# Kernel optimization log

Hardware: AMD Instinct MI355X
Metric: run time of the kernel (lower is better)

The kernel has to match this reference:

```python
import jax, jax.numpy as jnp
import numpy as np

BN_EPS = 1e-5
KNN_K = 9
HEAD = 4


def _bn(x, gamma, beta, axis=1):
    # eval-mode BatchNorm with running_mean=0, running_var=1
    shape = [1] * x.ndim
    shape[axis] = -1
    scale = (gamma / jnp.sqrt(1.0 + BN_EPS)).reshape(shape)
    return x * scale + beta.reshape(shape)


def _conv1d(x, W, b):
    # 1x1 Conv1d == channel matmul; x: [B,C,N], W: [O,C], b: [O]
    return jnp.einsum('oc,bcn->bon', W, x) + b[None, :, None]


def _knn_idx(x, k):
    # x: [B,C,N] -> idx [B,N,k] of k nearest (incl. self)
    xx = jnp.sum(x * x, axis=1)                      # [B,N]
    inner = jnp.einsum('bcn,bcm->bnm', x, x)         # [B,N,N]
    neg_d = 2.0 * inner - xx[:, :, None] - xx[:, None, :]
    return jax.lax.top_k(neg_d, k)[1]


def _graph_feature(x, k):
    # x: [B,C,N] -> [B,2C,N,k]  (cat of center feature and center - neighbor)
    B, C, N = x.shape
    idx = _knn_idx(x, k)                             # [B,N,k]
    xt = jnp.transpose(x, (0, 2, 1))                 # [B,N,C]
    nbr = jax.vmap(lambda xb, ib: xb[ib])(xt, idx)   # [B,N,k,C]
    ctr = jnp.broadcast_to(xt[:, :, None, :], (B, N, k, C))
    feat = jnp.concatenate([ctr, ctr - nbr], axis=3)  # [B,N,k,2C]
    return jnp.transpose(feat, (0, 3, 1, 2))


def _dgcnn_max(x, w1, b1, g1, be1, w2, b2, g2, be2, k):
    # x: [B,C,N] -> [B,C,N]; two 1x1 convs + BN + ReLU then max over k
    ef = _graph_feature(x, k)                        # [B,2C,N,k]
    h = jnp.einsum('oc,bcnk->bonk', w1, ef) + b1[None, :, None, None]
    h = jax.nn.relu(_bn(h, g1, be1, axis=1))
    h = jnp.einsum('oc,bcnk->bonk', w2, h) + b2[None, :, None, None]
    h = jax.nn.relu(_bn(h, g2, be2, axis=1))
    return jnp.max(h, axis=-1)                       # [B,C,N]


def _attention(m1, m2, wq, bq, wk, bk, wv, bv, wmh, bmh, wc1, bc1, cg, cbe, wc2, bc2):
    B, C, N = m1.shape
    hd = C // HEAD
    q = _conv1d(m1, wq, bq).reshape(B, HEAD, hd, N)
    kk = _conv1d(m2, wk, bk).reshape(B, HEAD, hd, -1)
    v = _conv1d(m2, wv, bv).reshape(B, HEAD, hd, -1)
    score = jax.nn.softmax(jnp.einsum('bhdn,bhdm->bhnm', q, kk) / (float(hd) ** 0.5), axis=-1)
    add = jnp.einsum('bhnm,bhdm->bhdn', score, v).reshape(B, C, N)
    add = _conv1d(add, wmh, bmh)
    cat = jnp.concatenate([m1, add], axis=1)         # [B,2C,N]
    h = jax.nn.relu(_bn(_conv1d(cat, wc1, bc1), cg, cbe, axis=1))
    return m1 + _conv1d(h, wc2, bc2)


def setup_inputs() -> dict:
    key = jax.random.key(0)
    B, C, N = 4, 128, 2000
    ks = jax.random.split(key, 24)

    def w(k, shape, s=0.05):
        return jax.random.normal(k, shape, dtype=jnp.float32) * s

    inp = {
        'x': jax.random.normal(ks[0], (B, C, N, 1), dtype=jnp.float32),
        'y': jax.random.normal(ks[1], (B, C, N), dtype=jnp.float32),
        # DGCNN_MAX_Block conv params (two 1x1 Conv2d + BN)
        'dg_w1': w(ks[2], (C, 2 * C)), 'dg_b1': w(ks[3], (C,)),
        'dg_g1': jnp.ones((C,), jnp.float32), 'dg_be1': jnp.zeros((C,), jnp.float32),
        'dg_w2': w(ks[4], (C, C)), 'dg_b2': w(ks[5], (C,)),
        'dg_g2': jnp.ones((C,), jnp.float32), 'dg_be2': jnp.zeros((C,), jnp.float32),
        # AttentionPropagation params
        'wq': w(ks[6], (C, C)), 'bq': w(ks[7], (C,)),
        'wk': w(ks[8], (C, C)), 'bk': w(ks[9], (C,)),
        'wv': w(ks[10], (C, C)), 'bv': w(ks[11], (C,)),
        'wmh': w(ks[12], (C, C)), 'bmh': w(ks[13], (C,)),
        'wc1': w(ks[14], (2 * C, 2 * C)), 'bc1': w(ks[15], (2 * C,)),
        'cg': jnp.ones((2 * C,), jnp.float32), 'cbe': jnp.zeros((2 * C,), jnp.float32),
        'wc2': w(ks[16], (C, 2 * C)), 'bc2': w(ks[17], (C,)),
    }
    return inp


def reference(x, y, dg_w1, dg_b1, dg_g1, dg_be1, dg_w2, dg_b2, dg_g2, dg_be2,
              wq, bq, wk, bk, wv, bv, wmh, bmh, wc1, bc1, cg, cbe, wc2, bc2):
    feats = x[:, :, :, 0]                            # [B,C,N]
    agg = _dgcnn_max(feats, dg_w1, dg_b1, dg_g1, dg_be1,
                     dg_w2, dg_b2, dg_g2, dg_be2, KNN_K)
    out = _attention(agg, y, wq, bq, wk, bk, wv, bv, wmh, bmh,
                     wc1, bc1, cg, cbe, wc2, bc2)
    return out[:, :, :, None]                        # [B,C,N,1]
```

## Files before the change

### kernel.cpp

```cpp
#include <hip/hip_runtime.h>

#define BATCH 4
#define CH    128
#define NPTS  2000
#define KNN   9
#define NHEAD 4
#define HD    32

typedef unsigned short u16;
typedef __attribute__((ext_vector_type(4))) float f32x4;
typedef __attribute__((ext_vector_type(8))) short bf16x8;

#define OFF_XT    0
#define OFF_YT    1024000
#define OFF_PT    2048000
#define OFF_QT    3072000
#define OFF_AGG   4096000
#define OFF_MH    5120000
#define OFF_MISC  6144000
#define OFF_W1SUM (OFF_MISC)
#define OFF_W1B   (OFF_MISC+16384)
#define OFF_W2T   (OFF_MISC+32768)
#define OFF_WC1T  (OFF_MISC+114688)
#define OFF_B1F   (OFF_MISC+212992)
#define OFF_B2F   (OFF_MISC+213120)
#define OFF_BC1F  (OFF_MISC+213248)
#define OFF_XX    (OFF_MISC+213504)
#define OFF_IDX   (OFF_MISC+221504)

__device__ __forceinline__ u16 bf16rne(float v)
{
    unsigned u = __float_as_uint(v);
    return (u16)((u + 0x7fffu + ((u >> 16) & 1u)) >> 16);
}
__device__ __forceinline__ void bsplit(float v, u16& hi, u16& lo)
{
    unsigned u = __float_as_uint(v);
    unsigned h16 = (u + 0x7fffu + ((u >> 16) & 1u)) >> 16;
    float hf = __uint_as_float(h16 << 16);
    float lf = v - hf;
    unsigned ul = __float_as_uint(lf);
    hi = (u16)h16;
    lo = (u16)((ul + 0x7fffu + ((ul >> 16) & 1u)) >> 16);
}

__device__ __forceinline__ f32x4 mfma16(bf16x8 a, bf16x8 b, f32x4 c)
{
    return __builtin_amdgcn_mfma_f32_16x16x32_bf16(a, b, c, 0, 0, 0);
}

__global__ __launch_bounds__(256) void prep_kernel(
    const float* __restrict__ w1, const float* __restrict__ b1,
    const float* __restrict__ g1, const float* __restrict__ be1,
    const float* __restrict__ w2, const float* __restrict__ b2,
    const float* __restrict__ g2, const float* __restrict__ be2,
    const float* __restrict__ wc1, const float* __restrict__ bc1,
    const float* __restrict__ cg, const float* __restrict__ cbe,
    float* __restrict__ ws)
{
    int id = blockIdx.x * 256 + threadIdx.x;
    const float rs = rsqrtf(1.f + 1e-5f);
    if (id < 16384) {
        int o = id >> 7, c = id & 127;
        float s1 = g1[o] * rs;
        ws[OFF_W1SUM + id] = (w1[o*256 + c] + w1[o*256 + 128 + c]) * s1;
        ws[OFF_W1B   + id] = w1[o*256 + 128 + c] * s1;
        ws[OFF_W2T   + id] = w2[id] * (g2[o] * rs);
    }
    {
        int o = id >> 8;
        ws[OFF_WC1T + id] = wc1[id] * (cg[o] * rs);
    }
    if (id < 128) {
        float s1 = g1[id] * rs, s2 = g2[id] * rs;
        ws[OFF_B1F + id] = b1[id]*s1 + be1[id];
        ws[OFF_B2F + id] = b2[id]*s2 + be2[id];
    }
    if (id < 256) {
        ws[OFF_BC1F + id] = bc1[id]*(cg[id]*rs) + cbe[id];
    }
}

__global__ __launch_bounds__(128) void transpose_kernel(
    const float* __restrict__ src, float* __restrict__ dst, float* __restrict__ xx)
{
    int blk = blockIdx.x; int b = blk / NPTS, n = blk % NPTS;
    int c = threadIdx.x;
    float v = src[((size_t)b*CH + c)*NPTS + n];
    dst[((size_t)b*NPTS + n)*CH + c] = v;
    if (xx) {
        __shared__ float red[128];
        red[c] = v*v;
        __syncthreads();
        for (int s = 64; s > 0; s >>= 1) { if (c < s) red[c] += red[c+s]; __syncthreads(); }
        if (c == 0) xx[b*NPTS + n] = red[0];
    }
}

__global__ __launch_bounds__(512) void knn8_kernel(
    const u16* __restrict__ XH, const u16* __restrict__ XL,
    const float* __restrict__ xx, int* __restrict__ idxOut)
{
    __shared__ float woutv[8][16][9];
    __shared__ int   wouti[8][16][9];
    int b = blockIdx.y;
    int q0 = blockIdx.x * 16;
    int tid = threadIdx.x;
    int wave = tid >> 6, lane = tid & 63;
    int lg = lane >> 4, lr = lane & 15;
    const float* xxb = xx + (size_t)b*NPTS;

    size_t qb = ((size_t)b*NPTS + q0 + lr)*128 + lg*8;
    bf16x8 qh[4], ql[4];
#pragma unroll
    for (int ch = 0; ch < 4; ch++) {
        qh[ch] = *(const bf16x8*)&XH[qb + ch*32];
        ql[ch] = *(const bf16x8*)&XL[qb + ch*32];
    }

    float vals[4][9]; int ids[4][9];
    float vmin[4]; int amin[4];
#pragma unroll
    for (int j = 0; j < 4; j++) {
#pragma unroll
        for (int k = 0; k < 9; k++) { vals[j][k] = -3.4e38f; ids[j][k] = -1; }
        vmin[j] = -3.4e38f; amin[j] = 0;
    }

    for (int t = wave; t < 125; t += 8) {
        size_t kb = ((size_t)b*NPTS + t*16 + lr)*128 + lg*8;
        bf16x8 fh[4], fl[4];
#pragma unroll
        for (int ch = 0; ch < 4; ch++) {
            fh[ch] = *(const bf16x8*)&XH[kb + ch*32];
            fl[ch] = *(const bf16x8*)&XL[kb + ch*32];
        }
        float xv = xxb[t*16 + lr];
        f32x4 acc = {0.f,0.f,0.f,0.f};
#pragma unroll
        for (int ch = 0; ch < 4; ch++) {
            acc = mfma16(qh[ch], fh[ch], acc);
            acc = mfma16(qh[ch], fl[ch], acc);
            acc = mfma16(ql[ch], fh[ch], acc);
            acc = mfma16(ql[ch], fl[ch], acc);
        }
        int cand = t*16 + lr;
#pragma unroll
        for (int j = 0; j < 4; j++) {
            float s = 2.f*acc[j] - xv;
            if (s > vmin[j]) {
#pragma unroll
                for (int k = 0; k < 9; k++) {
                    bool sel = (k == amin[j]);
                    vals[j][k] = sel ? s    : vals[j][k];
                    ids[j][k]  = sel ? cand : ids[j][k];
                }
                vmin[j] = vals[j][0]; amin[j] = 0;
#pragma unroll
                for (int k = 1; k < 9; k++) {
                    bool lt = vals[j][k] < vmin[j];
                    vmin[j] = lt ? vals[j][k] : vmin[j];
                    amin[j] = lt ? k : amin[j];
                }
            }
        }
    }

#pragma unroll
    for (int j = 0; j < 4; j++) {
        unsigned used = 0;
        for (int r = 0; r < 9; r++) {
            float bv = -3.4e38f; int bm = -1;
#pragma unroll
            for (int k = 0; k < 9; k++) {
                bool ok = !(used & (1u << k)) && (vals[j][k] > bv);
                bv = ok ? vals[j][k] : bv;
                bm = ok ? ids[j][k]  : bm;
            }
            float v = bv; int mi = bm;
#pragma unroll
            for (int off = 1; off < 16; off <<= 1) {
                float ov = __shfl_xor(v, off);
                int  omi = __shfl_xor(mi, off);
                if (ov > v || (ov == v && omi >= 0 && omi < mi)) { v = ov; mi = omi; }
            }
#pragma unroll
            for (int k = 0; k < 9; k++) {
                if (ids[j][k] == mi) used |= (1u << k);
            }
            if (lr == 0) { woutv[wave][lg*4+j][r] = v; wouti[wave][lg*4+j][r] = mi; }
        }
    }
    __syncthreads();

    if (tid < 16) {
        float v0 = woutv[0][tid][0], v1 = woutv[1][tid][0], v2 = woutv[2][tid][0], v3 = woutv[3][tid][0];
        float v4 = woutv[4][tid][0], v5 = woutv[5][tid][0], v6 = woutv[6][tid][0], v7 = woutv[7][tid][0];
        int   i0 = wouti[0][tid][0], i1 = wouti[1][tid][0], i2 = wouti[2][tid][0], i3 = wouti[3][tid][0];
        int   i4 = wouti[4][tid][0], i5 = wouti[5][tid][0], i6 = wouti[6][tid][0], i7 = wouti[7][tid][0];
        int   p0 = 1, p1 = 1, p2 = 1, p3 = 1, p4 = 1, p5 = 1, p6 = 1, p7 = 1;
        int* op = idxOut + ((size_t)b*NPTS + q0 + tid)*KNN;
        for (int r = 0; r < 9; r++) {
            int w = 0; float bv = v0; int bi = i0;
            if (v1 > bv || (v1 == bv && i1 < bi)) { w = 1; bv = v1; bi = i1; }
            if (v2 > bv || (v2 == bv && i2 < bi)) { w = 2; bv = v2; bi = i2; }
            if (v3 > bv || (v3 == bv && i3 < bi)) { w = 3; bv = v3; bi = i3; }
            if (v4 > bv || (v4 == bv && i4 < bi)) { w = 4; bv = v4; bi = i4; }
            if (v5 > bv || (v5 == bv && i5 < bi)) { w = 5; bv = v5; bi = i5; }
            if (v6 > bv || (v6 == bv && i6 < bi)) { w = 6; bv = v6; bi = i6; }
            if (v7 > bv || (v7 == bv && i7 < bi)) { w = 7; bv = v7; bi = i7; }
            op[r] = bi;
            if (w == 0)      { v0 = (p0 < 9) ? woutv[0][tid][p0] : -3.4e38f; i0 = (p0 < 9) ? wouti[0][tid][p0] : 0x7fffffff; p0++; }
            else if (w == 1) { v1 = (p1 < 9) ? woutv[1][tid][p1] : -3.4e38f; i1 = (p1 < 9) ? wouti[1][tid][p1] : 0x7fffffff; p1++; }
            else if (w == 2) { v2 = (p2 < 9) ? woutv[2][tid][p2] : -3.4e38f; i2 = (p2 < 9) ? wouti[2][tid][p2] : 0x7fffffff; p2++; }
            else if (w == 3) { v3 = (p3 < 9) ? woutv[3][tid][p3] : -3.4e38f; i3 = (p3 < 9) ? wouti[3][tid][p3] : 0x7fffffff; p3++; }
            else if (w == 4) { v4 = (p4 < 9) ? woutv[4][tid][p4] : -3.4e38f; i4 = (p4 < 9) ? wouti[4][tid][p4] : 0x7fffffff; p4++; }
            else if (w == 5) { v5 = (p5 < 9) ? woutv[5][tid][p5] : -3.4e38f; i5 = (p5 < 9) ? wouti[5][tid][p5] : 0x7fffffff; p5++; }
            else if (w == 6) { v6 = (p6 < 9) ? woutv[6][tid][p6] : -3.4e38f; i6 = (p6 < 9) ? wouti[6][tid][p6] : 0x7fffffff; p6++; }
            else             { v7 = (p7 < 9) ? woutv[7][tid][p7] : -3.4e38f; i7 = (p7 < 9) ? wouti[7][tid][p7] : 0x7fffffff; p7++; }
        }
    }
}

__global__ __launch_bounds__(128) void gemm_dual_kernel(
    const float* __restrict__ In, const float* __restrict__ Wa, const float* __restrict__ Wb,
    const float* __restrict__ ba, const float* __restrict__ bb,
    float* __restrict__ OutA, float* __restrict__ OutB)
{
    __shared__ float in_lds[8][128];
    int row0 = blockIdx.x * 8, tid = threadIdx.x;
    const float* src = In + (size_t)row0 * 128;
    for (int i = tid; i < 1024; i += 128) ((float*)in_lds)[i] = src[i];
    __syncthreads();
    float accA[8], accB[8];
    float bA = ba ? ba[tid] : 0.f, bB = bb ? bb[tid] : 0.f;
#pragma unroll
    for (int j = 0; j < 8; j++) { accA[j] = bA; accB[j] = bB; }
    const float4* wra = (const float4*)(Wa + (size_t)tid * 128);
    const float4* wrb = (const float4*)(Wb + (size_t)tid * 128);
#pragma unroll 4
    for (int c4 = 0; c4 < 32; c4++) {
        float4 wa = wra[c4], wb = wrb[c4];
#pragma unroll
        for (int j = 0; j < 8; j++) {
            float4 xi = ((const float4*)&in_lds[j][0])[c4];
            accA[j] += xi.x*wa.x + xi.y*wa.y + xi.z*wa.z + xi.w*wa.w;
            accB[j] += xi.x*wb.x + xi.y*wb.y + xi.z*wb.z + xi.w*wb.w;
        }
    }
#pragma unroll
    for (int j = 0; j < 8; j++) {
        OutA[(size_t)(row0 + j)*128 + tid] = accA[j];
        OutB[(size_t)(row0 + j)*128 + tid] = accB[j];
    }
}

template<int CIN, int COUT, bool RELU, bool TRANSOUT, bool HASRES, bool CONCAT>
__global__ __launch_bounds__(COUT) void gemmT_kernel(
    const float* __restrict__ In, const float* __restrict__ In2,
    const float* __restrict__ Wt, const float* __restrict__ bias,
    const float* __restrict__ Res, float* __restrict__ Out)
{
    __shared__ float in_lds[8][CIN];
    int row0 = blockIdx.x * 8, tid = threadIdx.x;
    if (!CONCAT) {
        const float* src = In + (size_t)row0 * CIN;
        for (int i = tid; i < 8*CIN; i += COUT) ((float*)in_lds)[i] = src[i];
    } else {
        for (int i = tid; i < 8*128; i += COUT) {
            int j = i >> 7, c = i & 127;
            in_lds[j][c]       = In [(size_t)(row0 + j)*128 + c];
            in_lds[j][128 + c] = In2[(size_t)(row0 + j)*128 + c];
        }
    }
    __syncthreads();
    float acc[8];
    float b = bias ? bias[tid] : 0.f;
#pragma unroll
    for (int j = 0; j < 8; j++) acc[j] = b;
    const float4* wrow = (const float4*)(Wt + (size_t)tid * CIN);
#pragma unroll 4
    for (int c4 = 0; c4 < CIN/4; c4++) {
        float4 w = wrow[c4];
#pragma unroll
        for (int j = 0; j < 8; j++) {
            float4 xi = ((const float4*)&in_lds[j][0])[c4];
            acc[j] += xi.x*w.x + xi.y*w.y + xi.z*w.z + xi.w*w.w;
        }
    }
#pragma unroll
    for (int j = 0; j < 8; j++) {
        float v = acc[j];
        if (RELU) v = fmaxf(v, 0.f);
        size_t row = row0 + j;
        if (HASRES) v += Res[row*COUT + tid];
        if (!TRANSOUT) {
            Out[row*COUT + tid] = v;
        } else {
            int b_ = (int)(row / NPTS), n_ = (int)(row % NPTS);
            Out[((size_t)b_*COUT + tid)*NPTS + n_] = v;
        }
    }
}

__global__ __launch_bounds__(128) void edgeconv_kernel(
    const float* __restrict__ Pt, const float* __restrict__ Qt,
    const int* __restrict__ idx, const float* __restrict__ W2t,
    const float* __restrict__ b2f, float* __restrict__ Agg)
{
    int blk = blockIdx.x; int b = blk / NPTS, n = blk % NPTS;
    int o = threadIdx.x;
    __shared__ float r[9][128];
    __shared__ int mk[9];
    if (o < 9) mk[o] = idx[((size_t)b*NPTS + n)*KNN + o];
    __syncthreads();
    float p = Pt[((size_t)b*NPTS + n)*128 + o];
#pragma unroll
    for (int k = 0; k < 9; k++) {
        float q = Qt[((size_t)b*NPTS + mk[k])*128 + o];
        r[k][o] = fmaxf(p - q, 0.f);
    }
    __syncthreads();
    float acc[9];
#pragma unroll
    for (int k = 0; k < 9; k++) acc[k] = 0.f;
    const float4* w2row = (const float4*)(W2t + (size_t)o * 128);
#pragma unroll 2
    for (int c4 = 0; c4 < 32; c4++) {
        float4 w = w2row[c4];
#pragma unroll
        for (int k = 0; k < 9; k++) {
            float4 rv = ((const float4*)&r[k][0])[c4];
            acc[k] += rv.x*w.x + rv.y*w.y + rv.z*w.z + rv.w*w.w;
        }
    }
    float bb = b2f[o];
    float vmax = -3.4e38f;
#pragma unroll
    for (int k = 0; k < 9; k++) vmax = fmaxf(vmax, fmaxf(acc[k] + bb, 0.f));
    Agg[((size_t)b*NPTS + n)*128 + o] = vmax;
}

__global__ __launch_bounds__(256) void split_bf16_kernel(
    const float* __restrict__ src, u16* __restrict__ H, u16* __restrict__ L)
{
    int id = blockIdx.x * 256 + threadIdx.x;
    float v = src[id];
    u16 hi, lo;
    bsplit(v, hi, lo);
    H[id] = hi; L[id] = lo;
}

__global__ __launch_bounds__(256) void split_v_kernel(
    const float* __restrict__ VA, u16* __restrict__ VTH, u16* __restrict__ VTL)
{
    __shared__ float t[32][33];
    int b = blockIdx.z, c0 = blockIdx.y * 32, n0 = blockIdx.x * 32;
    int tid = threadIdx.x;
    int cc = tid & 31, rr = tid >> 5;
#pragma unroll
    for (int p = 0; p < 4; p++) {
        int n = n0 + rr + p*8;
        t[rr + p*8][cc] = (n < NPTS) ? VA[((size_t)b*NPTS + n)*128 + c0 + cc] : 0.f;
    }
    __syncthreads();
#pragma unroll
    for (int p = 0; p < 4; p++) {
        int c = c0 + rr + p*8;
        int n = n0 + cc;
        if (n < NPTS) {
            u16 hi, lo;
            bsplit(t[cc][rr + p*8], hi, lo);
            size_t o = ((size_t)b*128 + c)*NPTS + n;
            VTH[o] = hi; VTL[o] = lo;
        }
    }
}

#define PSTR 72
__global__ __launch_bounds__(256) void attn_mfma_kernel(
    const u16* __restrict__ QH, const u16* __restrict__ QL,
    const u16* __restrict__ KH, const u16* __restrict__ KL,
    const u16* __restrict__ VTH, const u16* __restrict__ VTL,
    float* __restrict__ Add)
{
    __shared__ alignas(16) u16 Ph[4][16][PSTR];
    int b = blockIdx.z, h = blockIdx.y;
    int wave = threadIdx.x >> 6, lane = threadIdx.x & 63;
    int lg = lane >> 4, lr = lane & 15;
    int q0 = blockIdx.x * 64 + wave * 16;
    if (q0 >= NPTS) return;

    size_t qb = ((size_t)b*NPTS + q0 + lr)*128 + h*32 + lg*8;
    const bf16x8 qh = *(const bf16x8*)&QH[qb];
    const bf16x8 ql = *(const bf16x8*)&QL[qb];

    f32x4 o0 = {0.f,0.f,0.f,0.f}, o1 = {0.f,0.f,0.f,0.f};
    float mrun[4], lsum[4];
#pragma unroll
    for (int r = 0; r < 4; r++) { mrun[r] = -3.0e38f; lsum[r] = 0.f; }
    const float sc = 0.17677669529663687f;
    int shsrc = ((lr >> 2) << 4) | (lr & 3);

    for (int ks = 0; ks < NPTS; ks += 32) {
        int r1 = ks + 16 + lr; if (r1 > NPTS-1) r1 = NPTS-1;
        size_t kb0 = ((size_t)b*NPTS + ks + lr)*128 + h*32 + lg*8;
        size_t kb1 = ((size_t)b*NPTS + r1)*128 + h*32 + lg*8;
        bf16x8 k0h = *(const bf16x8*)&KH[kb0];
        bf16x8 k0l = *(const bf16x8*)&KL[kb0];
        bf16x8 k1h = *(const bf16x8*)&KH[kb1];
        bf16x8 k1l = *(const bf16x8*)&KL[kb1];
        f32x4 s0 = {0.f,0.f,0.f,0.f}, s1 = {0.f,0.f,0.f,0.f};
        s0 = mfma16(qh, k0h, s0);
        s0 = mfma16(qh, k0l, s0);
        s0 = mfma16(ql, k0h, s0);
        s1 = mfma16(qh, k1h, s1);
        s1 = mfma16(qh, k1l, s1);
        s1 = mfma16(ql, k1h, s1);
        bool vk1 = (ks + 16 + lr) < NPTS;
        float mx[4];
#pragma unroll
        for (int r = 0; r < 4; r++) {
            float a  = s0[r]*sc;
            float a2 = vk1 ? s1[r]*sc : -3.0e38f;
            s0[r] = a; s1[r] = a2;
            mx[r] = fmaxf(a, a2);
        }
#pragma unroll
        for (int off = 1; off < 16; off <<= 1) {
#pragma unroll
            for (int r = 0; r < 4; r++) mx[r] = fmaxf(mx[r], __shfl_xor(mx[r], off));
        }
        float e0[4], e1[4], rsu[4], sca[4];
#pragma unroll
        for (int r = 0; r < 4; r++) {
            float mn = fmaxf(mrun[r], mx[r]);
            sca[r] = __expf(mrun[r] - mn);
            mrun[r] = mn;
            e0[r] = __expf(s0[r] - mn);
            e1[r] = __expf(s1[r] - mn);
            rsu[r] = e0[r] + e1[r];
        }
#pragma unroll
        for (int off = 1; off < 16; off <<= 1) {
#pragma unroll
            for (int r = 0; r < 4; r++) rsu[r] += __shfl_xor(rsu[r], off);
        }
#pragma unroll
        for (int r = 0; r < 4; r++) lsum[r] = lsum[r]*sca[r] + rsu[r];
#pragma unroll
        for (int r = 0; r < 4; r++) {
            int qr = lg*4 + r;
            Ph[wave][qr][lr]      = bf16rne(e0[r]);
            Ph[wave][qr][16 + lr] = bf16rne(e1[r]);
        }
        float scsel = (lr & 2) ? ((lr & 1) ? sca[3] : sca[2])
                               : ((lr & 1) ? sca[1] : sca[0]);
        float osc = __shfl(scsel, shsrc);
#pragma unroll
        for (int r = 0; r < 4; r++) { o0[r] *= osc; o1[r] *= osc; }
        int cb = ks + lg*8; if (cb > NPTS-8) cb = NPTS-8;
        bf16x8 pbh = *(const bf16x8*)&Ph[wave][lr][lg*8];
        size_t vb = ((size_t)b*128 + h*32 + lr)*NPTS + cb;
        bf16x8 v0h = *(const bf16x8*)&VTH[vb];
        bf16x8 v0l = *(const bf16x8*)&VTL[vb];
        bf16x8 v1h = *(const bf16x8*)&VTH[vb + 16*NPTS];
        bf16x8 v1l = *(const bf16x8*)&VTL[vb + 16*NPTS];
        o0 = mfma16(v0h, pbh, o0);
        o0 = mfma16(v0l, pbh, o0);
        o1 = mfma16(v1h, pbh, o1);
        o1 = mfma16(v1l, pbh, o1);
    }
    float lsel = (lr & 2) ? ((lr & 1) ? lsum[3] : lsum[2])
                          : ((lr & 1) ? lsum[1] : lsum[0]);
    float rinv = 1.f / __shfl(lsel, shsrc);
    int q = q0 + lr;
    size_t ob = ((size_t)b*NPTS + q)*128 + h*32;
#pragma unroll
    for (int r = 0; r < 4; r++) {
        Add[ob + lg*4 + r]      = o0[r]*rinv;
        Add[ob + 16 + lg*4 + r] = o1[r]*rinv;
    }
}

extern "C" void kernel_launch(void* const* d_in, const int* in_sizes, int n_in,
                              void* d_out, int out_size, void* d_ws, size_t ws_size,
                              hipStream_t stream)
{
    const float* x    = (const float*)d_in[0];
    const float* y    = (const float*)d_in[1];
    const float* w1   = (const float*)d_in[2];
    const float* b1   = (const float*)d_in[3];
    const float* g1   = (const float*)d_in[4];
    const float* be1  = (const float*)d_in[5];
    const float* w2   = (const float*)d_in[6];
    const float* b2   = (const float*)d_in[7];
    const float* g2   = (const float*)d_in[8];
    const float* be2  = (const float*)d_in[9];
    const float* wq   = (const float*)d_in[10];
    const float* bq   = (const float*)d_in[11];
    const float* wk   = (const float*)d_in[12];
    const float* bk   = (const float*)d_in[13];
    const float* wv   = (const float*)d_in[14];
    const float* bv   = (const float*)d_in[15];
    const float* wmh  = (const float*)d_in[16];
    const float* bmh  = (const float*)d_in[17];
    const float* wc1  = (const float*)d_in[18];
    const float* bc1  = (const float*)d_in[19];
    const float* cg   = (const float*)d_in[20];
    const float* cbe  = (const float*)d_in[21];
    const float* wc2  = (const float*)d_in[22];
    const float* bc2  = (const float*)d_in[23];
    float* ws = (float*)d_ws;
    float* out = (float*)d_out;

    float* XT  = ws + OFF_XT;
    float* YT  = ws + OFF_YT;
    float* PT  = ws + OFF_PT;
    float* QT  = ws + OFF_QT;
    float* AGG = ws + OFF_AGG;
    float* MH  = ws + OFF_MH;
    float* XX  = ws + OFF_XX;
    int*   IDX = (int*)(ws + OFF_IDX);
    float* QA  = PT;
    float* KA  = PT;
    float* VA  = XT;
    float* ADD = YT;
    float* TT  = PT;
    const int SPE = BATCH*NPTS*CH;
    u16* XHs = (u16*)MH;  u16* XLs = XHs + SPE;
    u16* QHs = (u16*)MH;  u16* QLs = QHs + SPE;
    u16* KHs = (u16*)QT;  u16* KLs = KHs + SPE;
    u16* VTH = (u16*)PT;  u16* VTL = VTH + SPE;

    prep_kernel<<<256, 256, 0, stream>>>(w1, b1, g1, be1, w2, b2, g2, be2,
                                         wc1, bc1, cg, cbe, ws);
    transpose_kernel<<<BATCH*NPTS, 128, 0, stream>>>(x, XT, XX);
    transpose_kernel<<<BATCH*NPTS, 128, 0, stream>>>(y, YT, nullptr);
    split_bf16_kernel<<<SPE/256, 256, 0, stream>>>(XT, XHs, XLs);
    knn8_kernel<<<dim3(NPTS/16, BATCH), 512, 0, stream>>>(XHs, XLs, XX, IDX);
    gemm_dual_kernel<<<BATCH*NPTS/8, 128, 0, stream>>>(XT, ws + OFF_W1SUM, ws + OFF_W1B,
                                                       ws + OFF_B1F, nullptr, PT, QT);
    edgeconv_kernel<<<BATCH*NPTS, 128, 0, stream>>>(PT, QT, IDX, ws + OFF_W2T,
                                                    ws + OFF_B2F, AGG);
    gemmT_kernel<128,128,false,false,false,false><<<BATCH*NPTS/8, 128, 0, stream>>>(
        AGG, nullptr, wq, bq, nullptr, QA);
    split_bf16_kernel<<<SPE/256, 256, 0, stream>>>(QA, QHs, QLs);
    gemm_dual_kernel<<<BATCH*NPTS/8, 128, 0, stream>>>(YT, wk, wv, bk, bv, KA, VA);
    split_bf16_kernel<<<SPE/256, 256, 0, stream>>>(KA, KHs, KLs);
    split_v_kernel<<<dim3(63, 128/32, BATCH), 256, 0, stream>>>(VA, VTH, VTL);
    attn_mfma_kernel<<<dim3(32, NHEAD, BATCH), 256, 0, stream>>>(
        QHs, QLs, KHs, KLs, VTH, VTL, ADD);
    gemmT_kernel<128,128,false,false,false,false><<<BATCH*NPTS/8, 128, 0, stream>>>(
        ADD, nullptr, wmh, bmh, nullptr, MH);
    gemmT_kernel<256,256,true,false,false,true><<<BATCH*NPTS/8, 256, 0, stream>>>(
        AGG, MH, ws + OFF_WC1T, ws + OFF_BC1F, nullptr, TT);
    gemmT_kernel<256,128,false,true,true,false><<<BATCH*NPTS/8, 128, 0, stream>>>(
        TT, nullptr, wc2, bc2, AGG, out);
}
```

Measured before the change: 582.0 us.

## Fuse bf16 hi/lo splitting into producer kernels and widen attention key tiles

The standalone split_bf16 and split_v kernels go away. The hi/lo bf16 split now happens in the epilogues of the transpose, the Q projection and the K/V projection GEMMs, and V is written transposed straight from the GEMM. This removes several full read/write passes over fp32 intermediates and three kernel launches. The attention kernel now handles 64 keys per iteration instead of 32 and adds a low-part correction term for P (a Pl LDS buffer and an extra MFMA per tile), which raises accuracy but adds MFMA work and LDS traffic. The V-transposed stores from the GEMM are strided, which may reduce store efficiency.

```diff
diff --git a/kernel.cpp b/kernel.cpp
--- a/kernel.cpp
+++ b/kernel.cpp
@@ -28,11 +28,6 @@
 #define OFF_XX    (OFF_MISC+213504)
 #define OFF_IDX   (OFF_MISC+221504)
 
-__device__ __forceinline__ u16 bf16rne(float v)
-{
-    unsigned u = __float_as_uint(v);
-    return (u16)((u + 0x7fffu + ((u >> 16) & 1u)) >> 16);
-}
 __device__ __forceinline__ void bsplit(float v, u16& hi, u16& lo)
 {
     unsigned u = __float_as_uint(v);
@@ -81,20 +76,31 @@
     }
 }
 
-__global__ __launch_bounds__(128) void transpose_kernel(
-    const float* __restrict__ src, float* __restrict__ dst, float* __restrict__ xx)
+__global__ __launch_bounds__(128) void transpose_split_kernel(
+    const float* __restrict__ src, float* __restrict__ dst, float* __restrict__ xx,
+    u16* __restrict__ H, u16* __restrict__ L)
 {
     int blk = blockIdx.x; int b = blk / NPTS, n = blk % NPTS;
     int c = threadIdx.x;
     float v = src[((size_t)b*CH + c)*NPTS + n];
-    dst[((size_t)b*NPTS + n)*CH + c] = v;
-    if (xx) {
-        __shared__ float red[128];
-        red[c] = v*v;
-        __syncthreads();
-        for (int s = 64; s > 0; s >>= 1) { if (c < s) red[c] += red[c+s]; __syncthreads(); }
-        if (c == 0) xx[b*NPTS + n] = red[0];
-    }
+    size_t di = ((size_t)b*NPTS + n)*CH + c;
+    dst[di] = v;
+    u16 hi, lo;
+    bsplit(v, hi, lo);
+    H[di] = hi; L[di] = lo;
+    __shared__ float red[128];
+    red[c] = v*v;
+    __syncthreads();
+    for (int s = 64; s > 0; s >>= 1) { if (c < s) red[c] += red[c+s]; __syncthreads(); }
+    if (c == 0) xx[b*NPTS + n] = red[0];
+}
+
+__global__ __launch_bounds__(128) void transpose_kernel(
+    const float* __restrict__ src, float* __restrict__ dst)
+{
+    int blk = blockIdx.x; int b = blk / NPTS, n = blk % NPTS;
+    int c = threadIdx.x;
+    dst[((size_t)b*NPTS + n)*CH + c] = src[((size_t)b*CH + c)*NPTS + n];
 }
 
 __global__ __launch_bounds__(512) void knn8_kernel(
@@ -255,6 +261,78 @@
     }
 }
 
+__global__ __launch_bounds__(128) void gemm_kv_kernel(
+    const float* __restrict__ In, const float* __restrict__ Wa, const float* __restrict__ Wb,
+    const float* __restrict__ ba, const float* __restrict__ bb,
+    u16* __restrict__ KHo, u16* __restrict__ KLo,
+    u16* __restrict__ VTHo, u16* __restrict__ VTLo)
+{
+    __shared__ float in_lds[8][128];
+    int row0 = blockIdx.x * 8, tid = threadIdx.x;
+    const float* src = In + (size_t)row0 * 128;
+    for (int i = tid; i < 1024; i += 128) ((float*)in_lds)[i] = src[i];
+    __syncthreads();
+    float accA[8], accB[8];
+    float bA = ba[tid], bB = bb[tid];
+#pragma unroll
+    for (int j = 0; j < 8; j++) { accA[j] = bA; accB[j] = bB; }
+    const float4* wra = (const float4*)(Wa + (size_t)tid * 128);
+    const float4* wrb = (const float4*)(Wb + (size_t)tid * 128);
+#pragma unroll 4
+    for (int c4 = 0; c4 < 32; c4++) {
+        float4 wa = wra[c4], wb = wrb[c4];
+#pragma unroll
+        for (int j = 0; j < 8; j++) {
+            float4 xi = ((const float4*)&in_lds[j][0])[c4];
+            accA[j] += xi.x*wa.x + xi.y*wa.y + xi.z*wa.z + xi.w*wa.w;
+            accB[j] += xi.x*wb.x + xi.y*wb.y + xi.z*wb.z + xi.w*wb.w;
+        }
+    }
+    int b = row0 / NPTS, n0 = row0 % NPTS;
+#pragma unroll
+    for (int j = 0; j < 8; j++) {
+        u16 hh, ll;
+        bsplit(accA[j], hh, ll);
+        size_t ko = (size_t)(row0 + j)*128 + tid;
+        KHo[ko] = hh; KLo[ko] = ll;
+        bsplit(accB[j], hh, ll);
+        size_t vo = ((size_t)b*128 + tid)*NPTS + n0 + j;
+        VTHo[vo] = hh; VTLo[vo] = ll;
+    }
+}
+
+__global__ __launch_bounds__(128) void gemm_q_kernel(
+    const float* __restrict__ In, const float* __restrict__ Wt, const float* __restrict__ bias,
+    u16* __restrict__ H, u16* __restrict__ L)
+{
+    __shared__ float in_lds[8][128];
+    int row0 = blockIdx.x * 8, tid = threadIdx.x;
+    const float* src = In + (size_t)row0 * 128;
+    for (int i = tid; i < 1024; i += 128) ((float*)in_lds)[i] = src[i];
+    __syncthreads();
+    float acc[8];
+    float b = bias[tid];
+#pragma unroll
+    for (int j = 0; j < 8; j++) acc[j] = b;
+    const float4* wrow = (const float4*)(Wt + (size_t)tid * 128);
+#pragma unroll 4
+    for (int c4 = 0; c4 < 32; c4++) {
+        float4 w = wrow[c4];
+#pragma unroll
+        for (int j = 0; j < 8; j++) {
+            float4 xi = ((const float4*)&in_lds[j][0])[c4];
+            acc[j] += xi.x*w.x + xi.y*w.y + xi.z*w.z + xi.w*w.w;
+        }
+    }
+#pragma unroll
+    for (int j = 0; j < 8; j++) {
+        u16 hh, ll;
+        bsplit(acc[j], hh, ll);
+        size_t o = (size_t)(row0 + j)*128 + tid;
+        H[o] = hh; L[o] = ll;
+    }
+}
+
 template<int CIN, int COUT, bool RELU, bool TRANSOUT, bool HASRES, bool CONCAT>
 __global__ __launch_bounds__(COUT) void gemmT_kernel(
     const float* __restrict__ In, const float* __restrict__ In2,
@@ -341,42 +419,6 @@
     Agg[((size_t)b*NPTS + n)*128 + o] = vmax;
 }
 
-__global__ __launch_bounds__(256) void split_bf16_kernel(
-    const float* __restrict__ src, u16* __restrict__ H, u16* __restrict__ L)
-{
-    int id = blockIdx.x * 256 + threadIdx.x;
-    float v = src[id];
-    u16 hi, lo;
-    bsplit(v, hi, lo);
-    H[id] = hi; L[id] = lo;
-}
-
-__global__ __launch_bounds__(256) void split_v_kernel(
-    const float* __restrict__ VA, u16* __restrict__ VTH, u16* __restrict__ VTL)
-{
-    __shared__ float t[32][33];
-    int b = blockIdx.z, c0 = blockIdx.y * 32, n0 = blockIdx.x * 32;
-    int tid = threadIdx.x;
-    int cc = tid & 31, rr = tid >> 5;
-#pragma unroll
-    for (int p = 0; p < 4; p++) {
-        int n = n0 + rr + p*8;
-        t[rr + p*8][cc] = (n < NPTS) ? VA[((size_t)b*NPTS + n)*128 + c0 + cc] : 0.f;
-    }
-    __syncthreads();
-#pragma unroll
-    for (int p = 0; p < 4; p++) {
-        int c = c0 + rr + p*8;
-        int n = n0 + cc;
-        if (n < NPTS) {
-            u16 hi, lo;
-            bsplit(t[cc][rr + p*8], hi, lo);
-            size_t o = ((size_t)b*128 + c)*NPTS + n;
-            VTH[o] = hi; VTL[o] = lo;
-        }
-    }
-}
-
 #define PSTR 72
 __global__ __launch_bounds__(256) void attn_mfma_kernel(
     const u16* __restrict__ QH, const u16* __restrict__ QL,
@@ -385,6 +427,7 @@
     float* __restrict__ Add)
 {
     __shared__ alignas(16) u16 Ph[4][16][PSTR];
+    __shared__ alignas(16) u16 Pl[4][16][PSTR];
     int b = blockIdx.z, h = blockIdx.y;
     int wave = threadIdx.x >> 6, lane = threadIdx.x & 63;
     int lg = lane >> 4, lr = lane & 15;
@@ -402,44 +445,55 @@
     const float sc = 0.17677669529663687f;
     int shsrc = ((lr >> 2) << 4) | (lr & 3);
 
-    for (int ks = 0; ks < NPTS; ks += 32) {
-        int r1 = ks + 16 + lr; if (r1 > NPTS-1) r1 = NPTS-1;
-        size_t kb0 = ((size_t)b*NPTS + ks + lr)*128 + h*32 + lg*8;
-        size_t kb1 = ((size_t)b*NPTS + r1)*128 + h*32 + lg*8;
-        bf16x8 k0h = *(const bf16x8*)&KH[kb0];
-        bf16x8 k0l = *(const bf16x8*)&KL[kb0];
-        bf16x8 k1h = *(const bf16x8*)&KH[kb1];
-        bf16x8 k1l = *(const bf16x8*)&KL[kb1];
-        f32x4 s0 = {0.f,0.f,0.f,0.f}, s1 = {0.f,0.f,0.f,0.f};
-        s0 = mfma16(qh, k0h, s0);
-        s0 = mfma16(qh, k0l, s0);
-        s0 = mfma16(ql, k0h, s0);
-        s1 = mfma16(qh, k1h, s1);
-        s1 = mfma16(qh, k1l, s1);
-        s1 = mfma16(ql, k1h, s1);
-        bool vk1 = (ks + 16 + lr) < NPTS;
+    for (int ks = 0; ks < NPTS; ks += 64) {
+        f32x4 st[4];
+        bool vk[4];
+#pragma unroll
+        for (int s = 0; s < 4; s++) {
+            int key = ks + s*16 + lr;
+            vk[s] = key < NPTS;
+            int kc = key > NPTS-1 ? NPTS-1 : key;
+            size_t kb = ((size_t)b*NPTS + kc)*128 + h*32 + lg*8;
+            bf16x8 kh_ = *(const bf16x8*)&KH[kb];
+            bf16x8 kl_ = *(const bf16x8*)&KL[kb];
+            f32x4 ss = {0.f,0.f,0.f,0.f};
+            ss = mfma16(qh, kh_, ss);
+            ss = mfma16(qh, kl_, ss);
+            ss = mfma16(ql, kh_, ss);
+            st[s] = ss;
+        }
         float mx[4];
 #pragma unroll
         for (int r = 0; r < 4; r++) {
-            float a  = s0[r]*sc;
-            float a2 = vk1 ? s1[r]*sc : -3.0e38f;
-            s0[r] = a; s1[r] = a2;
-            mx[r] = fmaxf(a, a2);
+            float m_ = -3.0e38f;
+#pragma unroll
+            for (int s = 0; s < 4; s++) {
+                float a = vk[s] ? st[s][r]*sc : -3.0e38f;
+                st[s][r] = a;
+                m_ = fmaxf(m_, a);
+            }
+            mx[r] = m_;
         }
 #pragma unroll
         for (int off = 1; off < 16; off <<= 1) {
 #pragma unroll
             for (int r = 0; r < 4; r++) mx[r] = fmaxf(mx[r], __shfl_xor(mx[r], off));
         }
-        float e0[4], e1[4], rsu[4], sca[4];
+        float sca[4], rsu[4];
+        float e[4][4];
 #pragma unroll
         for (int r = 0; r < 4; r++) {
             float mn = fmaxf(mrun[r], mx[r]);
             sca[r] = __expf(mrun[r] - mn);
             mrun[r] = mn;
-            e0[r] = __expf(s0[r] - mn);
-            e1[r] = __expf(s1[r] - mn);
-            rsu[r] = e0[r] + e1[r];
+            float su = 0.f;
+#pragma unroll
+            for (int s = 0; s < 4; s++) {
+                float ev = __expf(st[s][r] - mn);
+                e[s][r] = ev;
+                su += ev;
+            }
+            rsu[r] = su;
         }
 #pragma unroll
         for (int off = 1; off < 16; off <<= 1) {
@@ -451,25 +505,36 @@
 #pragma unroll
         for (int r = 0; r < 4; r++) {
             int qr = lg*4 + r;
-            Ph[wave][qr][lr]      = bf16rne(e0[r]);
-            Ph[wave][qr][16 + lr] = bf16rne(e1[r]);
+#pragma unroll
+            for (int s = 0; s < 4; s++) {
+                u16 hh, ll;
+                bsplit(e[s][r], hh, ll);
+                Ph[wave][qr][s*16 + lr] = hh;
+                Pl[wave][qr][s*16 + lr] = ll;
+            }
         }
         float scsel = (lr & 2) ? ((lr & 1) ? sca[3] : sca[2])
                                : ((lr & 1) ? sca[1] : sca[0]);
         float osc = __shfl(scsel, shsrc);
 #pragma unroll
         for (int r = 0; r < 4; r++) { o0[r] *= osc; o1[r] *= osc; }
-        int cb = ks + lg*8; if (cb > NPTS-8) cb = NPTS-8;
-        bf16x8 pbh = *(const bf16x8*)&Ph[wave][lr][lg*8];
-        size_t vb = ((size_t)b*128 + h*32 + lr)*NPTS + cb;
-        bf16x8 v0h = *(const bf16x8*)&VTH[vb];
-        bf16x8 v0l = *(const bf16x8*)&VTL[vb];
-        bf16x8 v1h = *(const bf16x8*)&VTH[vb + 16*NPTS];
-        bf16x8 v1l = *(const bf16x8*)&VTL[vb + 16*NPTS];
-        o0 = mfma16(v0h, pbh, o0);
-        o0 = mfma16(v0l, pbh, o0);
-        o1 = mfma16(v1h, pbh, o1);
-        o1 = mfma16(v1l, pbh, o1);
+#pragma unroll
+        for (int c = 0; c < 2; c++) {
+            int cb = ks + c*32 + lg*8; if (cb > NPTS-8) cb = NPTS-8;
+            bf16x8 pbh = *(const bf16x8*)&Ph[wave][lr][c*32 + lg*8];
+            bf16x8 pbl = *(const bf16x8*)&Pl[wave][lr][c*32 + lg*8];
+            size_t vb = ((size_t)b*128 + h*32 + lr)*NPTS + cb;
+            bf16x8 v0h = *(const bf16x8*)&VTH[vb];
+            bf16x8 v0l = *(const bf16x8*)&VTL[vb];
+            bf16x8 v1h = *(const bf16x8*)&VTH[vb + 16*NPTS];
+            bf16x8 v1l = *(const bf16x8*)&VTL[vb + 16*NPTS];
+            o0 = mfma16(v0h, pbh, o0);
+            o0 = mfma16(v0l, pbh, o0);
+            o0 = mfma16(v0h, pbl, o0);
+            o1 = mfma16(v1h, pbh, o1);
+            o1 = mfma16(v1l, pbh, o1);
+            o1 = mfma16(v1h, pbl, o1);
+        }
     }
     float lsel = (lr & 2) ? ((lr & 1) ? lsum[3] : lsum[2])
                           : ((lr & 1) ? lsum[1] : lsum[0]);
@@ -522,9 +587,6 @@
     float* MH  = ws + OFF_MH;
     float* XX  = ws + OFF_XX;
     int*   IDX = (int*)(ws + OFF_IDX);
-    float* QA  = PT;
-    float* KA  = PT;
-    float* VA  = XT;
     float* ADD = YT;
     float* TT  = PT;
     const int SPE = BATCH*NPTS*CH;
@@ -535,20 +597,16 @@
 
     prep_kernel<<<256, 256, 0, stream>>>(w1, b1, g1, be1, w2, b2, g2, be2,
                                          wc1, bc1, cg, cbe, ws);
-    transpose_kernel<<<BATCH*NPTS, 128, 0, stream>>>(x, XT, XX);
-    transpose_kernel<<<BATCH*NPTS, 128, 0, stream>>>(y, YT, nullptr);
-    split_bf16_kernel<<<SPE/256, 256, 0, stream>>>(XT, XHs, XLs);
+    transpose_split_kernel<<<BATCH*NPTS, 128, 0, stream>>>(x, XT, XX, XHs, XLs);
+    transpose_kernel<<<BATCH*NPTS, 128, 0, stream>>>(y, YT);
     knn8_kernel<<<dim3(NPTS/16, BATCH), 512, 0, stream>>>(XHs, XLs, XX, IDX);
     gemm_dual_kernel<<<BATCH*NPTS/8, 128, 0, stream>>>(XT, ws + OFF_W1SUM, ws + OFF_W1B,
                                                        ws + OFF_B1F, nullptr, PT, QT);
     edgeconv_kernel<<<BATCH*NPTS, 128, 0, stream>>>(PT, QT, IDX, ws + OFF_W2T,
                                                     ws + OFF_B2F, AGG);
-    gemmT_kernel<128,128,false,false,false,false><<<BATCH*NPTS/8, 128, 0, stream>>>(
-        AGG, nullptr, wq, bq, nullptr, QA);
-    split_bf16_kernel<<<SPE/256, 256, 0, stream>>>(QA, QHs, QLs);
-    gemm_dual_kernel<<<BATCH*NPTS/8, 128, 0, stream>>>(YT, wk, wv, bk, bv, KA, VA);
-    split_bf16_kernel<<<SPE/256, 256, 0, stream>>>(KA, KHs, KLs);
-    split_v_kernel<<<dim3(63, 128/32, BATCH), 256, 0, stream>>>(VA, VTH, VTL);
+    gemm_q_kernel<<<BATCH*NPTS/8, 128, 0, stream>>>(AGG, wq, bq, QHs, QLs);
+    gemm_kv_kernel<<<BATCH*NPTS/8, 128, 0, stream>>>(YT, wk, wv, bk, bv,
+                                                     KHs, KLs, VTH, VTL);
     attn_mfma_kernel<<<dim3(32, NHEAD, BATCH), 256, 0, stream>>>(
         QHs, QLs, KHs, KLs, VTH, VTL, ADD);
     gemmT_kernel<128,128,false,false,false,false><<<BATCH*NPTS/8, 128, 0, stream>>>(
```

Result: faster. 569.0 us (-2.2%).
